# Kernel tuning notes

Hardware: AMD Instinct MI355X
Metric: run time of the kernel (lower is better)

The kernel has to match this reference:

```python
import jax, jax.numpy as jnp
import numpy as np

B, N, DIM = 1, 512, 1024
HEADS, DH = 16, 64          # dim_head = 64, _dim = heads*dh = 1024
P = 32                      # projection_dim
P2 = P // 2
NEG_INF = -1e30


def setup_inputs() -> dict:
    key = jax.random.key(0)
    ks = jax.random.split(key, 14)
    s = 0.02
    _dim = HEADS * DH
    return {
        "x":    jax.random.normal(ks[0], (B, N, DIM), dtype=jnp.float32),
        "Wqkv": jax.random.normal(ks[1], (3 * _dim, DIM), dtype=jnp.float32) * s,
        "Wout": jax.random.normal(ks[2], (DIM, _dim), dtype=jnp.float32) * s,
        "Wq":   jax.random.normal(ks[3], (P, DH), dtype=jnp.float32) * s,
        "bq":   jax.random.normal(ks[4], (P,), dtype=jnp.float32) * s,
        "Wk":   jax.random.normal(ks[5], (P, DH), dtype=jnp.float32) * s,
        "bk":   jax.random.normal(ks[6], (P,), dtype=jnp.float32) * s,
        "W1":   jax.random.normal(ks[7], (P, 2 * P), dtype=jnp.float32) * s,
        "b1":   jax.random.normal(ks[8], (P,), dtype=jnp.float32) * s,
        "W2":   jax.random.normal(ks[9], (P2, P), dtype=jnp.float32) * s,
        "b2":   jax.random.normal(ks[10], (P2,), dtype=jnp.float32) * s,
        "W3":   jax.random.normal(ks[11], (1, P2), dtype=jnp.float32) * s,
        "b3":   jax.random.normal(ks[12], (1,), dtype=jnp.float32) * s,
    }


def reference(x, Wqkv, Wout, Wq, bq, Wk, bk, W1, b1, W2, b2, W3, b3):
    b, n, _ = x.shape
    # qkv projection, then einops 'b n (d k h) -> k b h n d' split (d outermost!)
    qkv = jnp.einsum('bnc,oc->bno', x, Wqkv).reshape(b, n, DH, 3, HEADS)
    q = jnp.transpose(qkv[:, :, :, 0, :], (0, 3, 1, 2))  # [b,h,n,dh]
    k = jnp.transpose(qkv[:, :, :, 1, :], (0, 3, 1, 2))
    v = jnp.transpose(qkv[:, :, :, 2, :], (0, 3, 1, 2))

    qp = jnp.einsum('bhnd,pd->bhnp', q, Wq) + bq  # [b,h,n,P]
    kp = jnp.einsum('bhnd,pd->bhnp', k, Wk) + bk

    # linear1 on concat(q_i, k_j): split W1 -> broadcast-add (same math,
    # avoids materializing the [b,h,n,n,2P] concat tensor)
    W1q, W1k = W1[:, :P], W1[:, P:]
    a = jnp.einsum('bhnp,qp->bhnq', qp, W1q)      # [b,h,n,P]
    c = jnp.einsum('bhnp,qp->bhnq', kp, W1k)      # [b,h,n,P]
    h1 = jax.nn.relu(a[:, :, :, None, :] + c[:, :, None, :, :] + b1)  # [b,h,n,n,P]
    h2 = jax.nn.relu(jnp.einsum('bhijp,qp->bhijq', h1, W2) + b2)      # [b,h,n,n,P/2]
    score = jnp.einsum('bhijq,oq->bhijo', h2, W3)[..., 0] + b3[0]     # [b,h,n,n]

    # causal mask (triu(1) filled with -inf)
    i = jnp.arange(n)
    causal = i[None, :] > i[:, None]
    score = jnp.where(causal, NEG_INF, score)

    attn = jax.nn.softmax(score, axis=-1)
    out = jnp.einsum('bhij,bhjd->bhid', attn, v)                      # [b,h,n,dh]
    out = jnp.transpose(out, (0, 2, 1, 3)).reshape(b, n, HEADS * DH)  # b n (h d)
    return jnp.einsum('bne,oe->bno', out, Wout)
```

## Files before the change

kernel.cpp:

```cpp
#include <hip/hip_runtime.h>
#include <hip/hip_bf16.h>
#include <hip/hip_fp16.h>
#include <math.h>

#define N_SEQ 512
#define DIM   1024
#define HEADS 16
#define DH    64
#define P     32
#define P2    16
#define PSTR  520

typedef short    bf16x8 __attribute__((ext_vector_type(8)));
typedef _Float16 f16x8  __attribute__((ext_vector_type(8)));
typedef float    f32x4  __attribute__((ext_vector_type(4)));

__device__ inline unsigned short f2bf(float f) {
  union { float f; unsigned u; } v; v.f = f;
  unsigned r = (v.u + 0x7fffu + ((v.u >> 16) & 1u)) >> 16;
  return (unsigned short)r;
}

union H8 { f16x8 v; __half2 h2[4]; unsigned u32[4]; };

__global__ __launch_bounds__(256) void prep(
    const float* __restrict__ Wqkv, const float* __restrict__ Wq,
    const float* __restrict__ bq, const float* __restrict__ Wk,
    const float* __restrict__ bk, const float* __restrict__ W1,
    const float* __restrict__ b1,
    const float* __restrict__ x, const float* __restrict__ Wout,
    short* __restrict__ Wcomb, short* __restrict__ xb,
    short* __restrict__ Woutb, float* __restrict__ ba32,
    float* __restrict__ bc32) {
  const int b = blockIdx.x, tid = threadIdx.x;
  if (b < 256) {
    __shared__ float W1s[32][33];
    __shared__ float Wqs[32][65];
    __shared__ float wsm[32][65];
    __shared__ __align__(16) float qs[64][132];
    const int part = b >> 7, rem = b & 127;
    const int h = rem >> 3, c0 = (rem & 7) * 128;
    const int grow = part * 16 + h;
    for (int idx = tid; idx < 1024; idx += 256)
      W1s[idx >> 5][idx & 31] = W1[(idx >> 5) * 64 + part * 32 + (idx & 31)];
    const float* Wsel = part ? Wk : Wq;
    for (int idx = tid; idx < 2048; idx += 256)
      Wqs[idx >> 6][idx & 63] = Wsel[idx];
    for (int idx = tid; idx < 2048; idx += 256) {
      const int d = idx >> 5, c4 = idx & 31;
      *(float4*)&qs[d][c4 * 4] =
          *(const float4*)(Wqkv + (size_t)(d * 48 + grow) * DIM + c0 + c4 * 4);
    }
    __syncthreads();
    for (int idx = tid; idx < 2048; idx += 256) {
      const int q = idx >> 6, d = idx & 63;
      float s = 0.f;
#pragma unroll
      for (int p = 0; p < 32; ++p) s += W1s[q][p] * Wqs[p][d];
      wsm[q][d] = s;
    }
    __syncthreads();
    for (int idx = tid; idx < 4096; idx += 256) {
      const int q = idx >> 7, c = idx & 127;
      float s = 0.f;
#pragma unroll
      for (int d = 0; d < 64; ++d) s += wsm[q][d] * qs[d][c];
      Wcomb[(size_t)(part * 512 + h * 32 + q) * DIM + c0 + c] = (short)f2bf(s);
    }
    if (rem == 0 && tid < 32) {
      const float* bsel = part ? bk : bq;
      float s = 0.f;
#pragma unroll
      for (int p = 0; p < 32; ++p) s += W1s[tid][p] * bsel[p];
      if (part) s += b1[tid];
      (part ? bc32 : ba32)[tid] = s;
    }
  } else if (b < 384) {
#pragma unroll
    for (int rr = 0; rr < 8; ++rr) {
      const int ov = (b - 256) * 8 + rr;
      const int h = ov >> 6, d = ov & 63;
      const float4 v = *(const float4*)(Wqkv + (size_t)(d * 48 + 32 + h) * DIM + tid * 4);
      ushort4 o;
      o.x = f2bf(v.x); o.y = f2bf(v.y); o.z = f2bf(v.z); o.w = f2bf(v.w);
      *(ushort4*)(Wcomb + (size_t)(1024 + ov) * DIM + tid * 4) = o;
    }
  } else if (b < 512) {
    const int idx = (b - 384) * 256 + tid;
#pragma unroll
    for (int u = 0; u < 4; ++u) {
      const int t = u * 32768 + idx;
      const float4 v = ((const float4*)x)[t];
      ushort4 o;
      o.x = f2bf(v.x); o.y = f2bf(v.y); o.z = f2bf(v.z); o.w = f2bf(v.w);
      ((ushort4*)xb)[t] = o;
    }
  } else {
    const int idx = (b - 512) * 256 + tid;
#pragma unroll
    for (int u = 0; u < 4; ++u) {
      const int t = u * 65536 + idx;
      const float4 v = ((const float4*)Wout)[t];
      ushort4 o;
      o.x = f2bf(v.x); o.y = f2bf(v.y); o.z = f2bf(v.z); o.w = f2bf(v.w);
      ((ushort4*)Woutb)[t] = o;
    }
  }
}

__global__ __launch_bounds__(512) void gemm_acv(
    const short* __restrict__ xb, const short* __restrict__ Wcomb,
    const float* __restrict__ ba32, const float* __restrict__ bc32,
    __half* __restrict__ a_buf, __half* __restrict__ cb_buf,
    __half* __restrict__ vT) {
  const int bb = blockIdx.x;
  const int tm = bb >> 5;
  const int tn = bb & 31;
  const int w = threadIdx.x >> 6;
  const int wm = w >> 1, wn = w & 1;
  const int lane = threadIdx.x & 63;
  const int m = lane & 15, quad = lane >> 4;

  const int row0 = tm * 64 + wm * 16;
  const int col0 = tn * 64 + wn * 32;

  const short* pa  = xb + (size_t)(row0 + m) * DIM + quad * 8;
  const short* pb0 = Wcomb + (size_t)(col0 + m) * DIM + quad * 8;
  const short* pb1 = pb0 + (size_t)16 * DIM;

  bf16x8 abuf[4], b0buf[4], b1buf[4];
#pragma unroll
  for (int j = 0; j < 4; ++j) {
    abuf[j]  = *(const bf16x8*)(pa  + j * 32);
    b0buf[j] = *(const bf16x8*)(pb0 + j * 32);
    b1buf[j] = *(const bf16x8*)(pb1 + j * 32);
  }

  f32x4 acc0 = {0.f, 0.f, 0.f, 0.f}, acc1 = {0.f, 0.f, 0.f, 0.f};

#pragma unroll
  for (int ko = 0; ko < 8; ++ko) {
#pragma unroll
    for (int j = 0; j < 4; ++j) {
      const int k = ko * 4 + j;
      const bf16x8 av  = abuf[j];
      const bf16x8 b0v = b0buf[j];
      const bf16x8 b1v = b1buf[j];
      if (k + 4 < 32) {
        abuf[j]  = *(const bf16x8*)(pa  + (k + 4) * 32);
        b0buf[j] = *(const bf16x8*)(pb0 + (k + 4) * 32);
        b1buf[j] = *(const bf16x8*)(pb1 + (k + 4) * 32);
      }
      acc0 = __builtin_amdgcn_mfma_f32_16x16x32_bf16(av, b0v, acc0, 0, 0, 0);
      acc1 = __builtin_amdgcn_mfma_f32_16x16x32_bf16(av, b1v, acc1, 0, 0, 0);
    }
  }

#pragma unroll
  for (int r = 0; r < 4; ++r) {
    const int n = row0 + quad * 4 + r;
#pragma unroll
    for (int half = 0; half < 2; ++half) {
      const int o = col0 + half * 16 + m;
      const float val = half ? acc1[r] : acc0[r];
      if (o < 512) {
        const int hh = o >> 5, q = o & 31;
        a_buf[((size_t)hh * N_SEQ + n) * P + q] = __float2half(val + ba32[q]);
      } else if (o < 1024) {
        const int oo = o - 512, hh = oo >> 5, q = oo & 31;
        cb_buf[((size_t)hh * N_SEQ + n) * P + q] = __float2half(val + bc32[q]);
      } else {
        const int ov = o - 1024, hh = ov >> 6, d = ov & 63;
        vT[((size_t)hh * DH + d) * N_SEQ + n] = __float2half(val);
      }
    }
  }
}

__device__ inline float rowscore(const H8& a, const H8& c, f16x8 w2f,
                                 f32x4 b2q, float4 w3q) {
  const f16x8 z = (f16x8)(_Float16)0;
  const f16x8 u = __builtin_elementwise_max(a.v + c.v, z);
  f32x4 acc = b2q;
  acc = __builtin_amdgcn_mfma_f32_16x16x32_f16(w2f, u, acc, 0, 0, 0);
  return fmaxf(acc[0], 0.f) * w3q.x + fmaxf(acc[1], 0.f) * w3q.y
       + fmaxf(acc[2], 0.f) * w3q.z + fmaxf(acc[3], 0.f) * w3q.w;
}

__device__ inline float quadreduce4(float p0, float p1, float p2, float p3,
                                    int quad) {
  const float sx = (quad & 1) ? p0 : p1;
  const float sy = (quad & 1) ? p2 : p3;
  const float rx = __shfl_xor(sx, 16);
  const float ry = __shfl_xor(sy, 16);
  const float aa = ((quad & 1) ? p1 : p0) + rx;
  const float bb = ((quad & 1) ? p3 : p2) + ry;
  const float sz = (quad & 2) ? aa : bb;
  const float rz = __shfl_xor(sz, 32);
  return ((quad & 2) ? bb : aa) + rz;
}

__global__ __launch_bounds__(512) void attn_fused(
    const __half* __restrict__ a_g, const __half* __restrict__ cb_g,
    const float* __restrict__ W2, const float* __restrict__ b2,
    const float* __restrict__ W3,
    const __half* __restrict__ vT, short* __restrict__ attnb) {
  const int p = blockIdx.x;
  const int h = blockIdx.y;
  const int tid = threadIdx.x;
  const int w = tid >> 6;
  const int lane = tid & 63;
  const int m = lane & 15, quad = lane >> 4;

  __shared__ __align__(16) __half probS[32][PSTR];
  __shared__ float invS[32];

  const int tlo = p, thi = 31 - p;
  const int nlo = p + 1, nhi = 32 - p;

  {
    const int g = w & 3;
    const int par = w >> 2;
    f16x8 w2f;
    {
      const float4* wp = (const float4*)(W2 + m * P + quad * 8);
      const float4 w0 = wp[0], w1 = wp[1];
      H8 uu;
      uu.h2[0] = __floats2half2_rn(w0.x, w0.y);
      uu.h2[1] = __floats2half2_rn(w0.z, w0.w);
      uu.h2[2] = __floats2half2_rn(w1.x, w1.y);
      uu.h2[3] = __floats2half2_rn(w1.z, w1.w);
      w2f = uu.v;
    }
    const float4 b2f = *(const float4*)(b2 + quad * 4);
    const f32x4 b2q = {b2f.x, b2f.y, b2f.z, b2f.w};
    const float4 w3q = *(const float4*)(W3 + quad * 4);

    H8 alo[4], ahi[4];
#pragma unroll
    for (int r = 0; r < 4; ++r) {
      alo[r].v = *(const f16x8*)(a_g + ((size_t)h * N_SEQ + tlo * 16 + 4 * g + r) * P + quad * 8);
      ahi[r].v = *(const f16x8*)(a_g + ((size_t)h * N_SEQ + thi * 16 + 4 * g + r) * P + quad * 8);
    }

    for (int jt = par; jt < nhi; jt += 2) {
      H8 cb;
      cb.v = *(const f16x8*)(cb_g + ((size_t)h * N_SEQ + jt * 16 + m) * P + quad * 8);
      const float q0 = rowscore(ahi[0], cb, w2f, b2q, w3q);
      const float q1 = rowscore(ahi[1], cb, w2f, b2q, w3q);
      const float q2 = rowscore(ahi[2], cb, w2f, b2q, w3q);
      const float q3 = rowscore(ahi[3], cb, w2f, b2q, w3q);
      const float fh = quadreduce4(q0, q1, q2, q3, quad);
      probS[16 + 4 * g + quad][jt * 16 + m] = __float2half(fh);
      if (jt < nlo) {
        const float s0 = rowscore(alo[0], cb, w2f, b2q, w3q);
        const float s1 = rowscore(alo[1], cb, w2f, b2q, w3q);
        const float s2 = rowscore(alo[2], cb, w2f, b2q, w3q);
        const float s3 = rowscore(alo[3], cb, w2f, b2q, w3q);
        const float fl = quadreduce4(s0, s1, s2, s3, quad);
        probS[4 * g + quad][jt * 16 + m] = __float2half(fl);
      }
    }
  }
  __syncthreads();

  {
    const int lr = tid >> 4;
    const int c  = tid & 15;
    const int gi = (lr < 16) ? (tlo * 16 + lr) : (thi * 16 + (lr - 16));
    float mx = -1e30f;
#pragma unroll
    for (int k = 0; k < 4; ++k) {
      const int c0 = k * 128 + c * 8;
      if (c0 > gi) break;
      H8 vv; vv.v = *(const f16x8*)&probS[lr][c0];
#pragma unroll
      for (int uu = 0; uu < 8; ++uu) {
        const float s = __half2float(vv.h2[uu >> 1].data[uu & 1]);
        if (c0 + uu <= gi) mx = fmaxf(mx, s);
      }
    }
#pragma unroll
    for (int msk = 1; msk < 16; msk <<= 1) mx = fmaxf(mx, __shfl_xor(mx, msk));
    float sum = 0.f;
#pragma unroll
    for (int k = 0; k < 4; ++k) {
      const int c0 = k * 128 + c * 8;
      H8 vv; vv.v = *(const f16x8*)&probS[lr][c0];
      H8 o;
#pragma unroll
      for (int uu = 0; uu < 4; ++uu) {
        float e0 = 0.f, e1 = 0.f;
        if (c0 + 2 * uu <= gi) {
          e0 = __expf(__half2float(vv.h2[uu].data[0]) - mx);
          if (c0 + 2 * uu + 1 <= gi)
            e1 = __expf(__half2float(vv.h2[uu].data[1]) - mx);
        }
        sum += e0 + e1;
        o.h2[uu] = __floats2half2_rn(e0, e1);
      }
      *(f16x8*)&probS[lr][c0] = o.v;
    }
#pragma unroll
    for (int msk = 1; msk < 16; msk <<= 1) sum += __shfl_xor(sum, msk);
    if (c == 0) invS[lr] = 1.f / sum;
  }
  __syncthreads();

  {
    const int half = w >> 2;
    const int d0 = (w & 3) * 16;
    const __half* pb = vT + ((size_t)h * DH + d0 + m) * N_SEQ + quad * 8;
    const int lbase = half ? 16 : 0;
    const int tile = half ? thi : tlo;
    const int nk = half ? ((33 - p) >> 1) : ((p + 2) >> 1);
    f32x4 acc = {0.f, 0.f, 0.f, 0.f};
    for (int k = 0; k < nk; ++k) {
      const f16x8 aa = *(const f16x8*)&probS[lbase + m][k * 32 + quad * 8];
      const f16x8 bb = *(const f16x8*)(pb + k * 32);
      acc = __builtin_amdgcn_mfma_f32_16x16x32_f16(aa, bb, acc, 0, 0, 0);
    }
#pragma unroll
    for (int r = 0; r < 4; ++r) {
      const int lrow = quad * 4 + r;
      const float val = acc[r] * invS[lbase + lrow];
      attnb[(size_t)(tile * 16 + lrow) * DIM + h * DH + d0 + m] = (short)f2bf(val);
    }
  }
}

__global__ __launch_bounds__(512) void gemm_out16(
    const short* __restrict__ A, const short* __restrict__ B,
    float* __restrict__ C) {
  const int bb = blockIdx.x;
  const int tm = bb >> 4;
  const int tn = bb & 15;
  const int w = threadIdx.x >> 6;
  const int wm = w & 1, wn = w >> 1;
  const int lane = threadIdx.x & 63;
  const int m = lane & 15, quad = lane >> 4;

  const int row0 = tm * 32 + wm * 16;
  const int col0 = tn * 64 + wn * 16;

  const short* pa = A + (size_t)(row0 + m) * DIM + quad * 8;
  const short* pb = B + (size_t)(col0 + m) * DIM + quad * 8;

  bf16x8 abuf[4], bbuf[4];
#pragma unroll
  for (int j = 0; j < 4; ++j) {
    abuf[j] = *(const bf16x8*)(pa + j * 32);
    bbuf[j] = *(const bf16x8*)(pb + j * 32);
  }

  f32x4 acc = {0.f, 0.f, 0.f, 0.f};
#pragma unroll
  for (int ko = 0; ko < 8; ++ko) {
#pragma unroll
    for (int j = 0; j < 4; ++j) {
      const int k = ko * 4 + j;
      const bf16x8 av = abuf[j];
      const bf16x8 bv = bbuf[j];
      if (k + 4 < 32) {
        abuf[j] = *(const bf16x8*)(pa + (k + 4) * 32);
        bbuf[j] = *(const bf16x8*)(pb + (k + 4) * 32);
      }
      acc = __builtin_amdgcn_mfma_f32_16x16x32_bf16(av, bv, acc, 0, 0, 0);
    }
  }

#pragma unroll
  for (int r = 0; r < 4; ++r)
    C[(size_t)(row0 + quad * 4 + r) * DIM + col0 + m] = acc[r];
}

extern "C" void kernel_launch(void* const* d_in, const int* in_sizes, int n_in,
                              void* d_out, int out_size, void* d_ws, size_t ws_size,
                              hipStream_t stream) {
  const float* x    = (const float*)d_in[0];
  const float* Wqkv = (const float*)d_in[1];
  const float* Wout = (const float*)d_in[2];
  const float* Wq   = (const float*)d_in[3];
  const float* bq   = (const float*)d_in[4];
  const float* Wk   = (const float*)d_in[5];
  const float* bk   = (const float*)d_in[6];
  const float* W1   = (const float*)d_in[7];
  const float* b1   = (const float*)d_in[8];
  const float* W2   = (const float*)d_in[9];
  const float* b2   = (const float*)d_in[10];
  const float* W3   = (const float*)d_in[11];
  float* out = (float*)d_out;

  float*  ws     = (float*)d_ws;
  float*  ba32   = ws;
  float*  bc32   = ba32 + 32;
  __half* a_buf  = (__half*)(bc32 + 32);
  __half* cb_buf = a_buf + (size_t)HEADS * N_SEQ * P;
  __half* vT     = cb_buf + (size_t)HEADS * N_SEQ * P;
  short*  Wcomb  = (short*)(vT + (size_t)HEADS * DH * N_SEQ);
  short*  xb     = Wcomb + (size_t)2048 * DIM;
  short*  Woutb  = xb + (size_t)N_SEQ * DIM;
  short*  attnb  = Woutb + (size_t)DIM * DIM;

  prep<<<768, 256, 0, stream>>>(Wqkv, Wq, bq, Wk, bk, W1, b1, x, Wout,
                                Wcomb, xb, Woutb, ba32, bc32);

  gemm_acv<<<256, 512, 0, stream>>>(xb, Wcomb, ba32, bc32, a_buf, cb_buf, vT);

  dim3 g3(16, HEADS);
  attn_fused<<<g3, 512, 0, stream>>>(a_buf, cb_buf, W2, b2, W3, vT, attnb);

  gemm_out16<<<256, 512, 0, stream>>>(attnb, Woutb, out);
}
```

Before: 163.4 us.

## Split attention blocks per query tile and register-cache transposed Wqkv in prep

The attention kernel now launches one 256-thread block per 16-row query tile (32x16 grid) instead of pairing a low and high tile in a 512-thread block. Heads in the upper half reverse the tile order to mix heavy and light blocks. The loads of the next cb and V tiles are software-prefetched. The prep kernel stores the Wqkv slice transposed in shared memory and keeps one column in registers across 16 output rows, which cuts repeated LDS reads. Risks are load imbalance from uneven per-tile causal work and higher register pressure from the 64-float array.

```diff
diff --git a/kernel.cpp b/kernel.cpp
--- a/kernel.cpp
+++ b/kernel.cpp
@@ -37,7 +37,7 @@
     __shared__ float W1s[32][33];
     __shared__ float Wqs[32][65];
     __shared__ float wsm[32][65];
-    __shared__ __align__(16) float qs[64][132];
+    __shared__ __align__(16) float qsT[128][65];
     const int part = b >> 7, rem = b & 127;
     const int h = rem >> 3, c0 = (rem & 7) * 128;
     const int grow = part * 16 + h;
@@ -48,8 +48,12 @@
       Wqs[idx >> 6][idx & 63] = Wsel[idx];
     for (int idx = tid; idx < 2048; idx += 256) {
       const int d = idx >> 5, c4 = idx & 31;
-      *(float4*)&qs[d][c4 * 4] =
+      const float4 v =
           *(const float4*)(Wqkv + (size_t)(d * 48 + grow) * DIM + c0 + c4 * 4);
+      qsT[c4 * 4 + 0][d] = v.x;
+      qsT[c4 * 4 + 1][d] = v.y;
+      qsT[c4 * 4 + 2][d] = v.z;
+      qsT[c4 * 4 + 3][d] = v.w;
     }
     __syncthreads();
     for (int idx = tid; idx < 2048; idx += 256) {
@@ -60,12 +64,21 @@
       wsm[q][d] = s;
     }
     __syncthreads();
-    for (int idx = tid; idx < 4096; idx += 256) {
-      const int q = idx >> 7, c = idx & 127;
-      float s = 0.f;
-#pragma unroll
-      for (int d = 0; d < 64; ++d) s += wsm[q][d] * qs[d][c];
-      Wcomb[(size_t)(part * 512 + h * 32 + q) * DIM + c0 + c] = (short)f2bf(s);
+    {
+      const int c = tid & 127;
+      float qr[64];
+#pragma unroll
+      for (int d4 = 0; d4 < 16; ++d4)
+        *(float4*)&qr[d4 * 4] = *(const float4*)&qsT[c][d4 * 4];
+#pragma unroll
+      for (int step = 0; step < 16; ++step) {
+        const int idx = step * 256 + tid;
+        const int q = idx >> 7;
+        float s = 0.f;
+#pragma unroll
+        for (int d = 0; d < 64; ++d) s += wsm[q][d] * qr[d];
+        Wcomb[(size_t)(part * 512 + h * 32 + q) * DIM + c0 + c] = (short)f2bf(s);
+      }
     }
     if (rem == 0 && tid < 32) {
       const float* bsel = part ? bk : bq;
@@ -200,27 +213,25 @@
   return ((quad & 2) ? bb : aa) + rz;
 }
 
-__global__ __launch_bounds__(512) void attn_fused(
+__global__ __launch_bounds__(256) void attn_fused(
     const __half* __restrict__ a_g, const __half* __restrict__ cb_g,
     const float* __restrict__ W2, const float* __restrict__ b2,
     const float* __restrict__ W3,
     const __half* __restrict__ vT, short* __restrict__ attnb) {
-  const int p = blockIdx.x;
-  const int h = blockIdx.y;
+  const int xx = blockIdx.x, yy = blockIdx.y;
+  const int t = (yy & 8) ? (31 - xx) : xx;
+  const int h = yy;
   const int tid = threadIdx.x;
   const int w = tid >> 6;
   const int lane = tid & 63;
   const int m = lane & 15, quad = lane >> 4;
 
-  __shared__ __align__(16) __half probS[32][PSTR];
-  __shared__ float invS[32];
-
-  const int tlo = p, thi = 31 - p;
-  const int nlo = p + 1, nhi = 32 - p;
+  __shared__ __align__(16) __half probS[16][PSTR];
+  __shared__ float invS[16];
+
+  const int nj = t + 1;
 
   {
-    const int g = w & 3;
-    const int par = w >> 2;
     f16x8 w2f;
     {
       const float4* wp = (const float4*)(W2 + m * P + quad * 8);
@@ -236,30 +247,24 @@
     const f32x4 b2q = {b2f.x, b2f.y, b2f.z, b2f.w};
     const float4 w3q = *(const float4*)(W3 + quad * 4);
 
-    H8 alo[4], ahi[4];
-#pragma unroll
-    for (int r = 0; r < 4; ++r) {
-      alo[r].v = *(const f16x8*)(a_g + ((size_t)h * N_SEQ + tlo * 16 + 4 * g + r) * P + quad * 8);
-      ahi[r].v = *(const f16x8*)(a_g + ((size_t)h * N_SEQ + thi * 16 + 4 * g + r) * P + quad * 8);
-    }
-
-    for (int jt = par; jt < nhi; jt += 2) {
-      H8 cb;
-      cb.v = *(const f16x8*)(cb_g + ((size_t)h * N_SEQ + jt * 16 + m) * P + quad * 8);
-      const float q0 = rowscore(ahi[0], cb, w2f, b2q, w3q);
-      const float q1 = rowscore(ahi[1], cb, w2f, b2q, w3q);
-      const float q2 = rowscore(ahi[2], cb, w2f, b2q, w3q);
-      const float q3 = rowscore(ahi[3], cb, w2f, b2q, w3q);
-      const float fh = quadreduce4(q0, q1, q2, q3, quad);
-      probS[16 + 4 * g + quad][jt * 16 + m] = __float2half(fh);
-      if (jt < nlo) {
-        const float s0 = rowscore(alo[0], cb, w2f, b2q, w3q);
-        const float s1 = rowscore(alo[1], cb, w2f, b2q, w3q);
-        const float s2 = rowscore(alo[2], cb, w2f, b2q, w3q);
-        const float s3 = rowscore(alo[3], cb, w2f, b2q, w3q);
-        const float fl = quadreduce4(s0, s1, s2, s3, quad);
-        probS[4 * g + quad][jt * 16 + m] = __float2half(fl);
-      }
+    H8 ar[4];
+#pragma unroll
+    for (int r = 0; r < 4; ++r)
+      ar[r].v = *(const f16x8*)(a_g + ((size_t)h * N_SEQ + t * 16 + 4 * w + r) * P + quad * 8);
+
+    const __half* cbbase = cb_g + ((size_t)h * N_SEQ + m) * P + quad * 8;
+    H8 cbn;
+    cbn.v = *(const f16x8*)cbbase;
+    for (int jt = 0; jt < nj; ++jt) {
+      const H8 cb = cbn;
+      if (jt + 1 < nj)
+        cbn.v = *(const f16x8*)(cbbase + (size_t)(jt + 1) * 16 * P);
+      const float s0 = rowscore(ar[0], cb, w2f, b2q, w3q);
+      const float s1 = rowscore(ar[1], cb, w2f, b2q, w3q);
+      const float s2 = rowscore(ar[2], cb, w2f, b2q, w3q);
+      const float s3 = rowscore(ar[3], cb, w2f, b2q, w3q);
+      const float fl = quadreduce4(s0, s1, s2, s3, quad);
+      probS[4 * w + quad][jt * 16 + m] = __float2half(fl);
     }
   }
   __syncthreads();
@@ -267,7 +272,7 @@
   {
     const int lr = tid >> 4;
     const int c  = tid & 15;
-    const int gi = (lr < 16) ? (tlo * 16 + lr) : (thi * 16 + (lr - 16));
+    const int gi = t * 16 + lr;
     float mx = -1e30f;
 #pragma unroll
     for (int k = 0; k < 4; ++k) {
@@ -308,23 +313,22 @@
   __syncthreads();
 
   {
-    const int half = w >> 2;
-    const int d0 = (w & 3) * 16;
+    const int d0 = w * 16;
     const __half* pb = vT + ((size_t)h * DH + d0 + m) * N_SEQ + quad * 8;
-    const int lbase = half ? 16 : 0;
-    const int tile = half ? thi : tlo;
-    const int nk = half ? ((33 - p) >> 1) : ((p + 2) >> 1);
+    const int nk = (t + 2) >> 1;
     f32x4 acc = {0.f, 0.f, 0.f, 0.f};
+    f16x8 vb = *(const f16x8*)pb;
     for (int k = 0; k < nk; ++k) {
-      const f16x8 aa = *(const f16x8*)&probS[lbase + m][k * 32 + quad * 8];
-      const f16x8 bb = *(const f16x8*)(pb + k * 32);
+      const f16x8 bb = vb;
+      if (k + 1 < nk) vb = *(const f16x8*)(pb + (k + 1) * 32);
+      const f16x8 aa = *(const f16x8*)&probS[m][k * 32 + quad * 8];
       acc = __builtin_amdgcn_mfma_f32_16x16x32_f16(aa, bb, acc, 0, 0, 0);
     }
 #pragma unroll
     for (int r = 0; r < 4; ++r) {
       const int lrow = quad * 4 + r;
-      const float val = acc[r] * invS[lbase + lrow];
-      attnb[(size_t)(tile * 16 + lrow) * DIM + h * DH + d0 + m] = (short)f2bf(val);
+      const float val = acc[r] * invS[lrow];
+      attnb[(size_t)(t * 16 + lrow) * DIM + h * DH + d0 + m] = (short)f2bf(val);
     }
   }
 }
@@ -407,8 +411,8 @@
 
   gemm_acv<<<256, 512, 0, stream>>>(xb, Wcomb, ba32, bc32, a_buf, cb_buf, vT);
 
-  dim3 g3(16, HEADS);
-  attn_fused<<<g3, 512, 0, stream>>>(a_buf, cb_buf, W2, b2, W3, vT, attnb);
+  dim3 g3(32, HEADS);
+  attn_fused<<<g3, 256, 0, stream>>>(a_buf, cb_buf, W2, b2, W3, vT, attnb);
 
   gemm_out16<<<256, 512, 0, stream>>>(attnb, Woutb, out);
 }
```

Result: faster. 160.0 us (-2.1%).
